# Kernel tuning notes

Hardware: AMD Instinct MI355X
Metric: run time of the kernel (lower is better)

Reference implementation:

```python
import math
import jax, jax.numpy as jnp
import numpy as np

NUM_BUCKETS = 32
MAX_DISTANCE = 128
N_HEADS = 16
D_KV = 64


def relative_position_bucket(rel_pos, num_buckets=NUM_BUCKETS, max_distance=MAX_DISTANCE):
    # bidirectional=True path of the original
    n = -rel_pos
    nb = num_buckets // 2
    ret = (n < 0).astype(jnp.int32) * nb
    n = jnp.abs(n)
    max_exact = nb // 2
    is_small = n < max_exact
    val_large = max_exact + (
        jnp.log(n.astype(jnp.float32) / max_exact)
        / math.log(max_distance / max_exact)
        * (nb - max_exact)
    ).astype(jnp.int32)
    val_large = jnp.minimum(val_large, nb - 1)
    return jnp.where(is_small, n, val_large) + ret


def setup_inputs() -> dict:
    key = jax.random.key(0)
    ks = jax.random.split(key, 6)
    B, S, D = 2, 2048, 1024
    inner = N_HEADS * D_KV  # 1024
    sc = 1.0 / math.sqrt(D)
    return {
        "x": jax.random.normal(ks[0], (B, S, D), dtype=jnp.float32),
        "Wq": jax.random.normal(ks[1], (D, inner), dtype=jnp.float32) * sc,
        "Wk": jax.random.normal(ks[2], (D, inner), dtype=jnp.float32) * sc,
        "Wv": jax.random.normal(ks[3], (D, inner), dtype=jnp.float32) * sc,
        "Wo": jax.random.normal(ks[4], (inner, D), dtype=jnp.float32) * sc,
        "rel_table": jax.random.normal(ks[5], (NUM_BUCKETS, N_HEADS), dtype=jnp.float32),
        "attention_mask": jnp.zeros((B, 1, 1, S), dtype=jnp.float32),
    }


def reference(x, Wq, Wk, Wv, Wo, rel_table, attention_mask):
    B, S, D = x.shape
    H, Dk = N_HEADS, D_KV

    q = (x @ Wq).reshape(B, S, H, Dk).transpose(0, 2, 1, 3)  # bhqd
    k = (x @ Wk).reshape(B, S, H, Dk).transpose(0, 2, 1, 3)
    v = (x @ Wv).reshape(B, S, H, Dk).transpose(0, 2, 1, 3)

    # NOTE: T5 attention has no 1/sqrt(d) scaling
    scores = jnp.einsum('bhqd,bhkd->bhqk', q.astype(jnp.float32), k.astype(jnp.float32))

    pos = jnp.arange(S)
    rel_pos = pos[None, :] - pos[:, None]  # [S,S] = k_pos - q_pos
    buckets = relative_position_bucket(rel_pos)
    position_bias = jnp.transpose(rel_table[buckets], (2, 0, 1))  # [H,S,S]

    scores = scores + position_bias[None, ...] + attention_mask
    weights = jax.nn.softmax(scores, axis=-1)
    out = jnp.einsum('bhqk,bhkd->bhqd', weights, v.astype(jnp.float32))
    out = out.transpose(0, 2, 1, 3).reshape(B, S, H * Dk).astype(x.dtype)
    out = out @ Wo
    return (out, position_bias)
```

## Files before the change

### kernel.cpp

```cpp
#include <hip/hip_runtime.h>
#include <hip/hip_bf16.h>
#include <math.h>
#include <stdint.h>

typedef __bf16 bf16_t;
typedef __attribute__((ext_vector_type(8))) __bf16 bf16x8;
typedef __attribute__((ext_vector_type(4))) float f32x4;
typedef float f32x4a __attribute__((ext_vector_type(4), aligned(4)));
typedef unsigned short u16;
typedef unsigned int u32;

#define DEV static __device__ __forceinline__
#define LOG2E 1.4426950408889634f

DEV u16 f2b(float f){ bf16_t h = (bf16_t)f; return __builtin_bit_cast(u16, h); }
DEV float b2f(u16 u){ bf16_t h = __builtin_bit_cast(bf16_t, u); return (float)h; }
DEV f32x4 mfma16(bf16x8 a, bf16x8 b, f32x4 c){
  return __builtin_amdgcn_mfma_f32_16x16x32_bf16(a, b, c, 0, 0, 0);
}

#if __has_builtin(__builtin_amdgcn_exp2f)
DEV float fexp2(float x){ return __builtin_amdgcn_exp2f(x); }
#else
DEV float fexp2(float x){ return exp2f(x); }
#endif

DEV void gld16(const void* g, void* l){
  __builtin_amdgcn_global_load_lds((const __attribute__((address_space(1))) u32*)g,
                                   (__attribute__((address_space(3))) u32*)l, 16, 0, 0);
}

DEV bf16x8 ldsA64(const u16* arr, int row, int ch){
  return *(const bf16x8*)&arr[row*64 + ((ch ^ (row&7))*8)];
}
DEV bf16x8 ldsA32(const u16* arr, int row, int ch){
  return *(const bf16x8*)&arr[row*32 + ((ch ^ ((row>>1)&3))*8)];
}

__global__ __launch_bounds__(256) void k_prep(const float* __restrict__ x,
                                              const float* __restrict__ Wq, const float* __restrict__ Wk,
                                              const float* __restrict__ Wv, const float* __restrict__ Wo,
                                              const float* __restrict__ rel_table, const float* __restrict__ mask,
                                              u16* __restrict__ xh, u16* __restrict__ xl,
                                              u16* __restrict__ wth, u16* __restrict__ wot,
                                              float* __restrict__ bt, float* __restrict__ bt2,
                                              float* __restrict__ msk2){
  __shared__ float tile[64][65];
  int bid = blockIdx.x;
  int t = threadIdx.x;
  if(bid < 4096){
    size_t i = ((size_t)bid*256 + t)*4;
    float4 v = *(const float4*)(x + i);
    ushort4 hv, lv; float f, hf;
    f=v.x; hv.x=f2b(f); hf=b2f(hv.x); lv.x=f2b(f-hf);
    f=v.y; hv.y=f2b(f); hf=b2f(hv.y); lv.y=f2b(f-hf);
    f=v.z; hv.z=f2b(f); hf=b2f(hv.z); lv.z=f2b(f-hf);
    f=v.w; hv.w=f2b(f); hf=b2f(hv.w); lv.w=f2b(f-hf);
    *(ushort4*)(xh+i) = hv;
    *(ushort4*)(xl+i) = lv;
  } else if(bid < 5120){
    int rr = bid - 4096;
    int z = rr >> 8, ky = (rr >> 4) & 15, nx = rr & 15;
    const float* W = (z==0)?Wq:((z==1)?Wk:((z==2)?Wv:Wo));
    int n0 = nx*64, k0 = ky*64;
    int r = t>>6, c = t&63;
    #pragma unroll
    for(int i=0;i<16;i++){
      int row = i*4 + r;
      tile[row][c] = W[(size_t)(k0+row)*1024 + n0 + c];
    }
    __syncthreads();
    #pragma unroll
    for(int i=0;i<16;i++){
      int nrow = i*4 + r;
      float v = tile[c][nrow];
      size_t o = (size_t)(n0+nrow)*1024 + k0 + c;
      if(z<3) wth[(size_t)z*1048576 + o] = f2b(v);
      else    wot[o] = f2b(v);
    }
  } else {
    int gid = (bid-5120)*256 + t;
    if(gid < 4096) msk2[gid] = mask[gid]*LOG2E;
    int h = gid >> 12, idx = gid & 4095;
    float v = 0.f;
    if(idx < 4095){
      int delta = idx - 2047;
      int n = -delta;
      int ret = 0;
      if(n < 0){ ret = 16; n = -n; }
      int bucket;
      if(n < 8) bucket = n + ret;
      else {
        float a = (float)log((double)n * 0.125);
        float rr2 = (float)((double)a / (double)2.7725887298583984f);
        int vl = 8 + (int)(rr2 * 8.0f);
        vl = vl > 15 ? 15 : vl;
        bucket = vl + ret;
      }
      v = rel_table[bucket*16 + h];
    }
    bt[gid] = v;
    bt2[gid] = v*LOG2E - 32.0f;
  }
}

__global__ __launch_bounds__(256) void k_gemm_qkv(const u16* __restrict__ xh, const u16* __restrict__ xl,
                                                  const u16* __restrict__ wth,
                                                  u16* __restrict__ qh, u16* __restrict__ ql,
                                                  u16* __restrict__ kh, u16* __restrict__ vt){
  __shared__ __align__(16) u16 SM[17408];
  u16* Ah = SM; u16* Al = SM+4096; u16* Bh = SM+8192;
  int z = blockIdx.z;
  const u16* WH = wth + (size_t)z*1048576;
  int lin2 = blockIdx.x + 8*blockIdx.y;
  int nl2 = (lin2 & 7)*32 + (lin2 >> 3);
  int n0 = (nl2 & 7)*128, m0 = (nl2 >> 3)*128;
  int t = threadIdx.x, w = t>>6, lane = t&63, l16 = lane&15, g = lane>>4;
  f32x4 acc[4][4];
  #pragma unroll
  for(int i=0;i<4;i++)
    #pragma unroll
    for(int j=0;j<4;j++) acc[i][j] = {0.f,0.f,0.f,0.f};
  int rbase = (w>>1)*64, cbase = (w&1)*64;
  for(int k0=0;k0<1024;k0+=32){
    __syncthreads();
    #pragma unroll
    for(int jj=0;jj<6;jj++){
      int q = w + 4*jj;
      int arr = q>>3, sub = q&7;
      if(z!=0 && arr==1) continue;
      int row = sub*16 + (lane>>2);
      int lch = (lane&3) ^ ((row>>1)&3);
      const u16* src;
      if(arr==0)      src = xh + (size_t)(m0+row)*1024 + k0 + lch*8;
      else if(arr==1) src = xl + (size_t)(m0+row)*1024 + k0 + lch*8;
      else            src = WH + (size_t)(n0+row)*1024 + k0 + lch*8;
      gld16(src, &SM[q*512]);
    }
    __syncthreads();
    if(z!=0){
      bf16x8 ah[4];
      #pragma unroll
      for(int i=0;i<4;i++) ah[i] = ldsA32(Ah, rbase + i*16 + l16, g);
      #pragma unroll
      for(int j=0;j<4;j++){
        bf16x8 bh = ldsA32(Bh, cbase + j*16 + l16, g);
        #pragma unroll
        for(int i=0;i<4;i++)
          acc[i][j] = mfma16(ah[i], bh, acc[i][j]);
      }
    } else {
      bf16x8 ah[4], am[4];
      #pragma unroll
      for(int i=0;i<4;i++){
        int row = rbase + i*16 + l16;
        ah[i] = ldsA32(Ah, row, g);
        am[i] = ldsA32(Al, row, g);
      }
      #pragma unroll
      for(int j=0;j<4;j++){
        bf16x8 bh = ldsA32(Bh, cbase + j*16 + l16, g);
        #pragma unroll
        for(int i=0;i<4;i++){
          acc[i][j] = mfma16(ah[i], bh, acc[i][j]);
          acc[i][j] = mfma16(am[i], bh, acc[i][j]);
        }
      }
    }
  }
  if(z==2){
    __syncthreads();
    #pragma unroll
    for(int i=0;i<4;i++)
      #pragma unroll
      for(int j=0;j<4;j++)
        #pragma unroll
        for(int r=0;r<4;r++){
          int ml = rbase + i*16 + g*4 + r;
          int nl = cbase + j*16 + l16;
          SM[nl*136 + ml] = f2b(acc[i][j][r]);
        }
    __syncthreads();
    int bb = m0 >> 11;
    #pragma unroll
    for(int kk=0;kk<8;kk++){
      int id = t + 256*kk;
      int row = id>>4, ch = id&15;
      uint4 v = *(const uint4*)&SM[row*136 + ch*8];
      int n = n0 + row;
      size_t dst = ((size_t)(bb*16 + (n>>6))*64 + (n&63))*2048 + (m0&2047) + ch*8;
      *(uint4*)&vt[dst] = v;
    }
  } else {
    #pragma unroll
    for(int i=0;i<4;i++)
      #pragma unroll
      for(int j=0;j<4;j++)
        #pragma unroll
        for(int r=0;r<4;r++){
          int m = m0 + rbase + i*16 + g*4 + r;
          int n = n0 + cbase + j*16 + l16;
          float v = acc[i][j][r];
          if(z==0) v *= LOG2E;
          int b = m >> 11, s = m & 2047;
          int hh = n >> 6, d = n & 63;
          size_t a = ((size_t)(b*16+hh)*2048 + s)*64 + d;
          u16 hb = f2b(v);
          if(z==0){ qh[a]=hb; ql[a]=f2b(v - b2f(hb)); }
          else    { kh[a]=hb; }
        }
  }
}

__global__ __launch_bounds__(256,4) void k_attn(const u16* __restrict__ qh, const u16* __restrict__ ql,
                                              const u16* __restrict__ kh,
                                              const u16* __restrict__ vt, const float* __restrict__ bt2,
                                              const float* __restrict__ msk2,
                                              const float* __restrict__ bt, float* __restrict__ bias_out,
                                              u16* __restrict__ ao){
  __shared__ __align__(16) u16 SM[12800];
  u16* KH = SM; u16* VT = SM+4096;
  int lin = blockIdx.x + 32*blockIdx.y;
  int nlw = (lin & 7)*128 + (lin >> 3);
  int qx = nlw & 31, bh = nlw >> 5;
  int b = bh>>4, h = bh&15;
  int q0 = qx*64;
  int t = threadIdx.x, w = t>>6, lane = t&63, l16 = lane&15, g = lane>>4;
  size_t base  = (size_t)bh*2048*64;
  size_t vbase = (size_t)bh*64*2048;
  u16* PSw = SM + 8192 + w*1152;
  const float* bt2h = bt2 + h*4096;
  const float* msk2b = msk2 + b*2048;
  size_t wbase = ((size_t)(bh*32 + qx))*65536 + t*8;

  bf16x8 qfh[2], qfl[2];
  {
    int qr = q0 + w*16 + l16;
    size_t a0 = base + (size_t)qr*64 + g*8;
    qfh[0] = *(const bf16x8*)&qh[a0];
    qfl[0] = *(const bf16x8*)&ql[a0];
    qfh[1] = *(const bf16x8*)&qh[a0+32];
    qfl[1] = *(const bf16x8*)&ql[a0+32];
  }
  f32x4 O[4];
  float rs[4];
  #pragma unroll
  for(int jd=0;jd<4;jd++) O[jd] = {0.f,0.f,0.f,0.f};
  #pragma unroll
  for(int r=0;r<4;r++) rs[r] = 0.f;
  int qgbase = q0 + w*16 + g*4;

  f32x4a bv0, bv1;
  {
    size_t f = wbase;
    int hh = (int)(f >> 22);
    int rem = (int)(f & 4194303);
    int qq = rem >> 11;
    int kk = rem & 2047;
    const float* row = bt + hh*4096 + (kk - qq + 2047);
    bv0 = *(const f32x4a*)(row);
    bv1 = *(const f32x4a*)(row + 4);
  }

  for(int k0=0;k0<2048;k0+=64){
    __syncthreads();
    #pragma unroll
    for(int jj=0;jj<4;jj++){
      int q = w + 4*jj;
      int arr = q>>3, sub = q&7;
      int row = sub*8 + (lane>>3);
      int lch = (lane&7) ^ (row&7);
      const u16* src;
      if(arr==0) src = kh + base + (size_t)(k0+row)*64 + lch*8;
      else       src = vt + vbase + (size_t)row*2048 + k0 + lch*8;
      gld16(src, &SM[q*512]);
    }
    f32x4 sc[4];
    {
      const float* bb = bt2h + (k0 + l16 + 2047 - qgbase);
      #pragma unroll
      for(int j=0;j<4;j++){
        f32x4a ld = *(const f32x4a*)(bb + j*16 - 3);
        float mk = msk2b[k0 + j*16 + l16];
        sc[j] = (f32x4){ld[3]+mk, ld[2]+mk, ld[1]+mk, ld[0]+mk};
      }
    }
    __syncthreads();
    {
      size_t f = wbase + (size_t)(k0>>6)*2048;
      __builtin_nontemporal_store(bv0, (f32x4a*)(bias_out + f));
      __builtin_nontemporal_store(bv1, (f32x4a*)(bias_out + f + 4));
      if(k0 < 2048-64){
        size_t fn = f + 2048;
        int hh = (int)(fn >> 22);
        int rem = (int)(fn & 4194303);
        int qq = rem >> 11;
        int kk = rem & 2047;
        const float* row = bt + hh*4096 + (kk - qq + 2047);
        bv0 = *(const f32x4a*)(row);
        bv1 = *(const f32x4a*)(row + 4);
      }
    }
    __builtin_amdgcn_s_setprio(1);
    #pragma unroll
    for(int j=0;j<4;j++){
      int krow = j*16 + l16;
      bf16x8 kfh0 = ldsA64(KH, krow, g);
      bf16x8 kfh1 = ldsA64(KH, krow, 4+g);
      f32x4 s = sc[j];
      s = mfma16(qfh[0], kfh0, s);
      s = mfma16(qfl[0], kfh0, s);
      s = mfma16(qfh[1], kfh1, s);
      s = mfma16(qfl[1], kfh1, s);
      sc[j] = s;
    }
    __builtin_amdgcn_s_setprio(0);
    #pragma unroll
    for(int j=0;j<4;j++){
      #pragma unroll
      for(int r=0;r<4;r++){
        float p = fexp2(sc[j][r]);
        rs[r] += p;
        PSw[(g*4+r)*72 + j*16 + l16] = f2b(p);
      }
    }
    __builtin_amdgcn_s_setprio(1);
    #pragma unroll
    for(int ds=0; ds<2; ds++){
      bf16x8 pa = *(const bf16x8*)&PSw[l16*72 + ds*32 + g*8];
      #pragma unroll
      for(int jd=0;jd<4;jd++){
        bf16x8 vb = ldsA64(VT, jd*16 + l16, ds*4 + g);
        O[jd] = mfma16(pa, vb, O[jd]);
      }
    }
    __builtin_amdgcn_s_setprio(0);
  }
  #pragma unroll
  for(int r=0;r<4;r++){
    float v = rs[r];
    v += __shfl_xor(v,1,64);
    v += __shfl_xor(v,2,64);
    v += __shfl_xor(v,4,64);
    v += __shfl_xor(v,8,64);
    float inv = 1.f/v;
    int q = qgbase + r;
    size_t a = ((size_t)(b*2048 + q))*1024 + h*64;
    #pragma unroll
    for(int jd=0;jd<4;jd++)
      ao[a + jd*16 + l16] = f2b(O[jd][r]*inv);
  }
}

__global__ __launch_bounds__(256) void k_gemm_out(const u16* __restrict__ ao, const u16* __restrict__ wot,
                                                  float* __restrict__ out){
  __shared__ __align__(16) u16 SM[8192];
  u16* As = SM; u16* Bs = SM+4096;
  int lin2 = blockIdx.x + 8*blockIdx.y;
  int nl2 = (lin2 & 7)*32 + (lin2 >> 3);
  int n0 = (nl2 & 7)*128, m0 = (nl2 >> 3)*128;
  int t = threadIdx.x, w = t>>6, lane = t&63, l16 = lane&15, g = lane>>4;
  f32x4 acc[4][4];
  #pragma unroll
  for(int i=0;i<4;i++)
    #pragma unroll
    for(int j=0;j<4;j++) acc[i][j] = {0.f,0.f,0.f,0.f};
  int rbase = (w>>1)*64, cbase = (w&1)*64;
  for(int k0=0;k0<1024;k0+=32){
    __syncthreads();
    #pragma unroll
    for(int jj=0;jj<4;jj++){
      int q = w + 4*jj;
      int arr = q>>3, sub = q&7;
      int row = sub*16 + (lane>>2);
      int lch = (lane&3) ^ ((row>>1)&3);
      const u16* src;
      if(arr==0) src = ao  + (size_t)(m0+row)*1024 + k0 + lch*8;
      else       src = wot + (size_t)(n0+row)*1024 + k0 + lch*8;
      gld16(src, &SM[q*512]);
    }
    __syncthreads();
    bf16x8 af[4];
    #pragma unroll
    for(int i=0;i<4;i++) af[i] = ldsA32(As, rbase + i*16 + l16, g);
    #pragma unroll
    for(int j=0;j<4;j++){
      bf16x8 bfb = ldsA32(Bs, cbase + j*16 + l16, g);
      #pragma unroll
      for(int i=0;i<4;i++)
        acc[i][j] = mfma16(af[i], bfb, acc[i][j]);
    }
  }
  #pragma unroll
  for(int i=0;i<4;i++)
    #pragma unroll
    for(int j=0;j<4;j++)
      #pragma unroll
      for(int r=0;r<4;r++){
        int m = m0 + rbase + i*16 + g*4 + r;
        int n = n0 + cbase + j*16 + l16;
        __builtin_nontemporal_store(acc[i][j][r], &out[(size_t)m*1024 + n]);
      }
}

extern "C" void kernel_launch(void* const* d_in, const int* in_sizes, int n_in,
                              void* d_out, int out_size, void* d_ws, size_t ws_size,
                              hipStream_t stream) {
  const float* x   = (const float*)d_in[0];
  const float* Wq  = (const float*)d_in[1];
  const float* Wk  = (const float*)d_in[2];
  const float* Wv  = (const float*)d_in[3];
  const float* Wo  = (const float*)d_in[4];
  const float* rel = (const float*)d_in[5];
  const float* msk = (const float*)d_in[6];
  float* out = (float*)d_out;
  float* bias_out = out + (size_t)4194304;
  char* ws = (char*)d_ws;
  u16* xh  = (u16*)(ws + 0);
  u16* xl  = (u16*)(ws + 8388608);
  u16* wth = (u16*)(ws + 16777216);
  u16* wot = (u16*)(ws + 23068672);
  u16* qh  = (u16*)(ws + 25165824);
  u16* ql  = (u16*)(ws + 33554432);
  u16* kh  = (u16*)(ws + 41943040);
  u16* vt  = (u16*)(ws + 50331648);
  u16* ao  = (u16*)(ws + 58720256);
  float* bt  = (float*)(ws + 67108864);
  float* bt2 = (float*)(ws + 67371008);
  float* msk2= (float*)(ws + 67633152);

  k_prep      <<<5376, 256, 0, stream>>>(x, Wq, Wk, Wv, Wo, rel, msk,
                                         xh, xl, wth, wot, bt, bt2, msk2);
  k_gemm_qkv  <<<dim3(8,32,3), 256, 0, stream>>>(xh, xl, wth, qh, ql, kh, vt);
  k_attn      <<<dim3(32,32), 256, 0, stream>>>(qh, ql, kh, vt, bt2, msk2, bt, bias_out, ao);
  k_gemm_out  <<<dim3(8,32), 256, 0, stream>>>(ao, wot, out);
}
```

Before: 450.5 us.

## Double-buffer LDS tiles in QKV GEMM, attention, and output GEMM kernels

Each of the three main kernels now uses two LDS buffers. The loads for the next K-tile are issued before the MFMA work on the current tile, and the loop keeps one barrier per iteration instead of two. The aim is to hide global-to-LDS load latency behind compute. The attention kernel also swaps the padded P staging layout for an XOR-swizzled 64-wide layout to avoid LDS bank conflicts. The cost is more LDS per block, which may lower occupancy, especially for the attention kernel's 4-blocks-per-CU target.

```diff
diff --git a/kernel.cpp b/kernel.cpp
--- a/kernel.cpp
+++ b/kernel.cpp
@@ -108,8 +108,7 @@
                                                   const u16* __restrict__ wth,
                                                   u16* __restrict__ qh, u16* __restrict__ ql,
                                                   u16* __restrict__ kh, u16* __restrict__ vt){
-  __shared__ __align__(16) u16 SM[17408];
-  u16* Ah = SM; u16* Al = SM+4096; u16* Bh = SM+8192;
+  __shared__ __align__(16) u16 SM[24576];
   int z = blockIdx.z;
   const u16* WH = wth + (size_t)z*1048576;
   int lin2 = blockIdx.x + 8*blockIdx.y;
@@ -122,22 +121,44 @@
     #pragma unroll
     for(int j=0;j<4;j++) acc[i][j] = {0.f,0.f,0.f,0.f};
   int rbase = (w>>1)*64, cbase = (w&1)*64;
-  for(int k0=0;k0<1024;k0+=32){
-    __syncthreads();
-    #pragma unroll
-    for(int jj=0;jj<6;jj++){
-      int q = w + 4*jj;
-      int arr = q>>3, sub = q&7;
-      if(z!=0 && arr==1) continue;
-      int row = sub*16 + (lane>>2);
-      int lch = (lane&3) ^ ((row>>1)&3);
-      const u16* src;
-      if(arr==0)      src = xh + (size_t)(m0+row)*1024 + k0 + lch*8;
-      else if(arr==1) src = xl + (size_t)(m0+row)*1024 + k0 + lch*8;
-      else            src = WH + (size_t)(n0+row)*1024 + k0 + lch*8;
-      gld16(src, &SM[q*512]);
-    }
-    __syncthreads();
+
+  #pragma unroll
+  for(int jj=0;jj<6;jj++){
+    int q = w + 4*jj;
+    int arr = q>>3, sub = q&7;
+    if(z!=0 && arr==1) continue;
+    int row = sub*16 + (lane>>2);
+    int lch = (lane&3) ^ ((row>>1)&3);
+    const u16* src;
+    if(arr==0)      src = xh + (size_t)(m0+row)*1024 + lch*8;
+    else if(arr==1) src = xl + (size_t)(m0+row)*1024 + lch*8;
+    else            src = WH + (size_t)(n0+row)*1024 + lch*8;
+    gld16(src, &SM[q*512]);
+  }
+  __syncthreads();
+
+  for(int it=0; it<32; ++it){
+    const u16* Ah = SM + (it&1)*12288;
+    const u16* Al = Ah + 4096;
+    const u16* Bh = Ah + 8192;
+    if(it < 31){
+      u16* dstb = SM + ((it+1)&1)*12288;
+      int kn = (it+1)*32;
+      #pragma unroll
+      for(int jj=0;jj<6;jj++){
+        int q = w + 4*jj;
+        int arr = q>>3, sub = q&7;
+        if(z!=0 && arr==1) continue;
+        int row = sub*16 + (lane>>2);
+        int lch = (lane&3) ^ ((row>>1)&3);
+        const u16* src;
+        if(arr==0)      src = xh + (size_t)(m0+row)*1024 + kn + lch*8;
+        else if(arr==1) src = xl + (size_t)(m0+row)*1024 + kn + lch*8;
+        else            src = WH + (size_t)(n0+row)*1024 + kn + lch*8;
+        gld16(src, dstb + q*512);
+      }
+      __builtin_amdgcn_sched_barrier(0);
+    }
     if(z!=0){
       bf16x8 ah[4];
       #pragma unroll
@@ -167,9 +188,9 @@
         }
       }
     }
+    __syncthreads();
   }
   if(z==2){
-    __syncthreads();
     #pragma unroll
     for(int i=0;i<4;i++)
       #pragma unroll
@@ -218,8 +239,7 @@
                                               const float* __restrict__ msk2,
                                               const float* __restrict__ bt, float* __restrict__ bias_out,
                                               u16* __restrict__ ao){
-  __shared__ __align__(16) u16 SM[12800];
-  u16* KH = SM; u16* VT = SM+4096;
+  __shared__ __align__(16) u16 SM[20480];
   int lin = blockIdx.x + 32*blockIdx.y;
   int nlw = (lin & 7)*128 + (lin >> 3);
   int qx = nlw & 31, bh = nlw >> 5;
@@ -228,7 +248,7 @@
   int t = threadIdx.x, w = t>>6, lane = t&63, l16 = lane&15, g = lane>>4;
   size_t base  = (size_t)bh*2048*64;
   size_t vbase = (size_t)bh*64*2048;
-  u16* PSw = SM + 8192 + w*1152;
+  u16* PSw = SM + 16384 + w*1024;
   const float* bt2h = bt2 + h*4096;
   const float* msk2b = msk2 + b*2048;
   size_t wbase = ((size_t)(bh*32 + qx))*65536 + t*8;
@@ -261,19 +281,36 @@
     bv0 = *(const f32x4a*)(row);
     bv1 = *(const f32x4a*)(row + 4);
   }
-
-  for(int k0=0;k0<2048;k0+=64){
-    __syncthreads();
-    #pragma unroll
-    for(int jj=0;jj<4;jj++){
-      int q = w + 4*jj;
-      int arr = q>>3, sub = q&7;
-      int row = sub*8 + (lane>>3);
-      int lch = (lane&7) ^ (row&7);
-      const u16* src;
-      if(arr==0) src = kh + base + (size_t)(k0+row)*64 + lch*8;
-      else       src = vt + vbase + (size_t)row*2048 + k0 + lch*8;
-      gld16(src, &SM[q*512]);
+  #pragma unroll
+  for(int jj=0;jj<4;jj++){
+    int q = w + 4*jj;
+    int arr = q>>3, sub = q&7;
+    int row = sub*8 + (lane>>3);
+    int lch = (lane&7) ^ (row&7);
+    const u16* src = (arr==0) ? kh + base + (size_t)row*64 + lch*8
+                              : vt + vbase + (size_t)row*2048 + lch*8;
+    gld16(src, &SM[q*512]);
+  }
+  __syncthreads();
+
+  for(int it=0; it<32; ++it){
+    int k0 = it*64;
+    const u16* KH = SM + (it&1)*8192;
+    const u16* VT = KH + 4096;
+    if(it < 31){
+      u16* dstb = SM + ((it+1)&1)*8192;
+      int kn = k0 + 64;
+      #pragma unroll
+      for(int jj=0;jj<4;jj++){
+        int q = w + 4*jj;
+        int arr = q>>3, sub = q&7;
+        int row = sub*8 + (lane>>3);
+        int lch = (lane&7) ^ (row&7);
+        const u16* src = (arr==0) ? kh + base + (size_t)(kn+row)*64 + lch*8
+                                  : vt + vbase + (size_t)row*2048 + kn + lch*8;
+        gld16(src, dstb + q*512);
+      }
+      __builtin_amdgcn_sched_barrier(0);
     }
     f32x4 sc[4];
     {
@@ -285,12 +322,11 @@
         sc[j] = (f32x4){ld[3]+mk, ld[2]+mk, ld[1]+mk, ld[0]+mk};
       }
     }
-    __syncthreads();
     {
-      size_t f = wbase + (size_t)(k0>>6)*2048;
+      size_t f = wbase + (size_t)it*2048;
       __builtin_nontemporal_store(bv0, (f32x4a*)(bias_out + f));
       __builtin_nontemporal_store(bv1, (f32x4a*)(bias_out + f + 4));
-      if(k0 < 2048-64){
+      if(it < 31){
         size_t fn = f + 2048;
         int hh = (int)(fn >> 22);
         int rem = (int)(fn & 4194303);
@@ -321,13 +357,15 @@
       for(int r=0;r<4;r++){
         float p = fexp2(sc[j][r]);
         rs[r] += p;
-        PSw[(g*4+r)*72 + j*16 + l16] = f2b(p);
+        int rowp = g*4 + r;
+        int colp = j*16 + l16;
+        PSw[rowp*64 + (((colp>>3) ^ (rowp&7))*8) + (colp&7)] = f2b(p);
       }
     }
     __builtin_amdgcn_s_setprio(1);
     #pragma unroll
     for(int ds=0; ds<2; ds++){
-      bf16x8 pa = *(const bf16x8*)&PSw[l16*72 + ds*32 + g*8];
+      bf16x8 pa = ldsA64(PSw, l16, ds*4 + g);
       #pragma unroll
       for(int jd=0;jd<4;jd++){
         bf16x8 vb = ldsA64(VT, jd*16 + l16, ds*4 + g);
@@ -335,6 +373,7 @@
       }
     }
     __builtin_amdgcn_s_setprio(0);
+    __syncthreads();
   }
   #pragma unroll
   for(int r=0;r<4;r++){
@@ -354,8 +393,7 @@
 
 __global__ __launch_bounds__(256) void k_gemm_out(const u16* __restrict__ ao, const u16* __restrict__ wot,
                                                   float* __restrict__ out){
-  __shared__ __align__(16) u16 SM[8192];
-  u16* As = SM; u16* Bs = SM+4096;
+  __shared__ __align__(16) u16 SM[16384];
   int lin2 = blockIdx.x + 8*blockIdx.y;
   int nl2 = (lin2 & 7)*32 + (lin2 >> 3);
   int n0 = (nl2 & 7)*128, m0 = (nl2 >> 3)*128;
@@ -366,20 +404,37 @@
     #pragma unroll
     for(int j=0;j<4;j++) acc[i][j] = {0.f,0.f,0.f,0.f};
   int rbase = (w>>1)*64, cbase = (w&1)*64;
-  for(int k0=0;k0<1024;k0+=32){
-    __syncthreads();
-    #pragma unroll
-    for(int jj=0;jj<4;jj++){
-      int q = w + 4*jj;
-      int arr = q>>3, sub = q&7;
-      int row = sub*16 + (lane>>2);
-      int lch = (lane&3) ^ ((row>>1)&3);
-      const u16* src;
-      if(arr==0) src = ao  + (size_t)(m0+row)*1024 + k0 + lch*8;
-      else       src = wot + (size_t)(n0+row)*1024 + k0 + lch*8;
-      gld16(src, &SM[q*512]);
-    }
-    __syncthreads();
+
+  #pragma unroll
+  for(int jj=0;jj<4;jj++){
+    int q = w + 4*jj;
+    int arr = q>>3, sub = q&7;
+    int row = sub*16 + (lane>>2);
+    int lch = (lane&3) ^ ((row>>1)&3);
+    const u16* src = (arr==0) ? ao  + (size_t)(m0+row)*1024 + lch*8
+                              : wot + (size_t)(n0+row)*1024 + lch*8;
+    gld16(src, &SM[q*512]);
+  }
+  __syncthreads();
+
+  for(int it=0; it<32; ++it){
+    const u16* As = SM + (it&1)*8192;
+    const u16* Bs = As + 4096;
+    if(it < 31){
+      u16* dstb = SM + ((it+1)&1)*8192;
+      int kn = (it+1)*32;
+      #pragma unroll
+      for(int jj=0;jj<4;jj++){
+        int q = w + 4*jj;
+        int arr = q>>3, sub = q&7;
+        int row = sub*16 + (lane>>2);
+        int lch = (lane&3) ^ ((row>>1)&3);
+        const u16* src = (arr==0) ? ao  + (size_t)(m0+row)*1024 + kn + lch*8
+                                  : wot + (size_t)(n0+row)*1024 + kn + lch*8;
+        gld16(src, dstb + q*512);
+      }
+      __builtin_amdgcn_sched_barrier(0);
+    }
     bf16x8 af[4];
     #pragma unroll
     for(int i=0;i<4;i++) af[i] = ldsA32(As, rbase + i*16 + l16, g);
@@ -390,6 +445,7 @@
       for(int i=0;i<4;i++)
         acc[i][j] = mfma16(af[i], bfb, acc[i][j]);
     }
+    __syncthreads();
   }
   #pragma unroll
   for(int i=0;i<4;i++)
```

Measured after the change: 442.3 us. About the same (-1.8%).
